# Kernel optimization log

Hardware: AMD Instinct MI355X
Metric: run time of the kernel (lower is better)

Reference implementation:

```python
import jax, jax.numpy as jnp
import numpy as np

B = 4096
HASH_BITS = 128
TEACHER_DIM = 768
TEMPERATURE = 0.2
CONTRASTIVE_W = 1.0
DISTILL_W = 0.5
QUANT_W = 0.01


def _l2_normalize(x, eps=1e-12):
    # matches torch F.normalize(dim=-1)
    n = jnp.sqrt(jnp.sum(x * x, axis=-1, keepdims=True))
    return x / jnp.maximum(n, eps)


def setup_inputs() -> dict:
    key = jax.random.key(0)
    k1, k2, k3, k4 = jax.random.split(key, 4)
    logits = jax.random.normal(k1, (B, HASH_BITS), dtype=jnp.float32)
    # binary {-1,+1} codes as in the module contract
    hash_codes = jnp.sign(jax.random.normal(k2, (B, HASH_BITS), dtype=jnp.float32))
    hash_codes = jnp.where(hash_codes == 0, 1.0, hash_codes)
    teacher_embed = jax.random.normal(k3, (B, TEACHER_DIM), dtype=jnp.float32)
    # sparse random positives plus self-positives (guarantees each row nonempty)
    rand_pos = jax.random.uniform(k4, (B, B)) < 0.002
    eye = jnp.eye(B, dtype=bool)
    positive_mask = rand_pos | eye
    return {
        "logits": logits,
        "hash_codes": hash_codes,
        "teacher_embed": teacher_embed,
        "positive_mask": positive_mask,
    }


def reference(logits, hash_codes, teacher_embed, positive_mask):
    teacher = _l2_normalize(teacher_embed)

    # ---- contrastive (vectorized form of the per-row python loop) ----
    ln = _l2_normalize(logits)
    sim = (ln @ ln.T) / TEMPERATURE  # [B, B]
    eye = jnp.eye(sim.shape[0], dtype=bool)
    sim_masked = jnp.where(eye, -jnp.inf, sim)
    # per-row stable logsumexp over self-masked similarities
    log_denom = jax.nn.logsumexp(sim_masked, axis=1)  # [B]
    pm = positive_mask.astype(sim.dtype)
    cnt = pm.sum(axis=1)  # [B]
    pos_mean = (sim * pm).sum(axis=1) / jnp.maximum(cnt, 1.0)
    has_pos = cnt > 0
    per_row = jnp.where(has_pos, -pos_mean + log_denom, 0.0)
    num_pos = jnp.maximum(has_pos.sum(), 1)
    loss_cont = per_row.sum() / num_pos.astype(sim.dtype)

    # ---- distillation: hash similarity vs teacher similarity MSE ----
    hash_sim = (hash_codes @ hash_codes.T) / hash_codes.shape[-1]
    teacher_sim = teacher @ teacher.T
    loss_distill = jnp.mean((hash_sim - teacher_sim) ** 2)

    # ---- quantization: push |logits| toward 1 ----
    loss_quant = jnp.mean(jnp.abs(jnp.abs(logits) - 1.0))

    total = (
        CONTRASTIVE_W * loss_cont
        + DISTILL_W * loss_distill
        + QUANT_W * loss_quant
    )
    return total
```

## Files before the change

kernel.cpp:

```cpp
#include <hip/hip_runtime.h>


typedef unsigned short u16x8 __attribute__((ext_vector_type(8)));
typedef __bf16 bf16x8 __attribute__((ext_vector_type(8)));
typedef float f32x4 __attribute__((ext_vector_type(4)));

__device__ __forceinline__ unsigned short f2bf(float f) {
  union { float f; unsigned int u; } v; v.f = f;
  unsigned int u = v.u;
  return (unsigned short)((u + 0x7FFFu + ((u >> 16) & 1u)) >> 16);
}

__global__ __launch_bounds__(256) void prep(const float* __restrict__ logits,
                                            const float* __restrict__ hash,
                                            const float* __restrict__ teacher,
                                            unsigned short* __restrict__ P,
                                            float* __restrict__ qpart,
                                            float* __restrict__ rowexp,
                                            float* __restrict__ possum,
                                            float* __restrict__ cntw) {
  const int r = blockIdx.x, t = threadIdx.x;
  const int wave = t >> 6, lane = t & 63;
  __shared__ float s4[4], s2[2], q2[2];

  float x0 = teacher[(size_t)r * 768 + t];
  float x1 = teacher[(size_t)r * 768 + 256 + t];
  float x2 = teacher[(size_t)r * 768 + 512 + t];
  float ss = x0 * x0 + x1 * x1 + x2 * x2;
#pragma unroll
  for (int off = 1; off < 64; off <<= 1) ss += __shfl_xor(ss, off, 64);
  if (lane == 0) s4[wave] = ss;

  float xl = 0.f;
  if (t < 128) {
    xl = logits[(size_t)r * 128 + t];
    float ssl = xl * xl;
    float qv = fabsf(fabsf(xl) - 1.0f);
#pragma unroll
    for (int off = 1; off < 64; off <<= 1) {
      ssl += __shfl_xor(ssl, off, 64);
      qv += __shfl_xor(qv, off, 64);
    }
    if (lane == 0) { s2[wave] = ssl; q2[wave] = qv; }
  }
  __syncthreads();

  float rnt = 1.0f / fmaxf(sqrtf(s4[0] + s4[1] + s4[2] + s4[3]), 1e-12f);
  P[(size_t)r * 1024 + 256 + t] = f2bf(x0 * rnt);
  P[(size_t)r * 1024 + 512 + t] = f2bf(x1 * rnt);
  P[(size_t)r * 1024 + 768 + t] = f2bf(x2 * rnt);
  if (t < 128) {
    float rnl = 1.0f / fmaxf(sqrtf(s2[0] + s2[1]), 1e-12f);
    P[(size_t)r * 1024 + t] = f2bf(xl * rnl);
    P[(size_t)r * 1024 + 128 + t] =
        f2bf(hash[(size_t)r * 128 + t] * 0.08838834764831845f);
  }
  if (t == 0) {
    qpart[r] = q2[0] + q2[1];
    rowexp[r] = 0.f; possum[r] = 0.f; cntw[r] = 0.f;
  }
}

#define STAGE(KC)                                                              \
  {                                                                            \
    _Pragma("unroll") for (int it = 0; it < 4; ++it) {                         \
      const int seg = it * 4 + wave;                                           \
      const int row = seg * 4 + (lane >> 4);                                   \
      const int g = (lane & 15) ^ (row & 7);                                   \
      const unsigned short* gpA =                                              \
          P + (size_t)(ti + row) * 1024 + (KC) * 128 + g * 8;                  \
      __builtin_amdgcn_global_load_lds(                                        \
          (const __attribute__((address_space(1))) void*)gpA,                  \
          (__attribute__((address_space(3))) void*)&S[seg * 512], 16, 0, 0);   \
      if (offdiag) {                                                           \
        const unsigned short* gpB =                                            \
            P + (size_t)(tj + row) * 1024 + (KC) * 128 + g * 8;                \
        __builtin_amdgcn_global_load_lds(                                      \
            (const __attribute__((address_space(1))) void*)gpB,                \
            (__attribute__((address_space(3))) void*)&S[8192 + seg * 512],     \
            16, 0, 0);                                                         \
      }                                                                        \
    }                                                                          \
  }

#define CHUNK_MFMA(A0, A1, A2, A3)                                             \
  {                                                                            \
    _Pragma("unroll") for (int ks = 0; ks < 4; ++ks) {                         \
      const int gg = (ks * 4 + qd) ^ swz;                                      \
      bf16x8 af = *(const bf16x8*)&S[(wave * 16 + l15) * 128 + gg * 8];        \
      bf16x8 b0 = *(const bf16x8*)&S[boff + l15 * 128 + gg * 8];               \
      A0 = __builtin_amdgcn_mfma_f32_16x16x32_bf16(af, b0, A0, 0, 0, 0);       \
      bf16x8 b1 = *(const bf16x8*)&S[boff + (16 + l15) * 128 + gg * 8];        \
      A1 = __builtin_amdgcn_mfma_f32_16x16x32_bf16(af, b1, A1, 0, 0, 0);       \
      bf16x8 b2 = *(const bf16x8*)&S[boff + (32 + l15) * 128 + gg * 8];        \
      A2 = __builtin_amdgcn_mfma_f32_16x16x32_bf16(af, b2, A2, 0, 0, 0);       \
      bf16x8 b3 = *(const bf16x8*)&S[boff + (48 + l15) * 128 + gg * 8];        \
      A3 = __builtin_amdgcn_mfma_f32_16x16x32_bf16(af, b3, A3, 0, 0, 0);       \
    }                                                                          \
  }

__global__ __launch_bounds__(256) void hash_main(const unsigned short* __restrict__ P,
                                                 const void* __restrict__ mask,
                                                 float* __restrict__ rowexp,
                                                 float* __restrict__ possum,
                                                 float* __restrict__ cntw,
                                                 float* __restrict__ dpart) {
  const int b = (int)blockIdx.x;
  const int l = (b & 7) * 260 + (b >> 3);
  int bi = (int)((129.0f - sqrtf(16641.0f - 8.0f * (float)l)) * 0.5f);
  while (bi * (129 - bi) / 2 > l) --bi;
  while ((bi + 1) * (128 - bi) / 2 <= l) ++bi;
  const int bj = bi + (l - bi * (129 - bi) / 2);
  const int ti = bi * 64, tj = bj * 64;
  const bool offdiag = (bi != bj);

  const int t = threadIdx.x;
  const int wave = t >> 6, lane = t & 63;
  const int qd = lane >> 4, l15 = lane & 15;
  const int swz = l15 & 7;

  __shared__ __align__(16) unsigned short S[16384];
  __shared__ float red[4];
  const int boff = offdiag ? 8192 : 0;

  f32x4 s0 = {0.f, 0.f, 0.f, 0.f}, s1 = s0, s2 = s0, s3 = s0;
  f32x4 d0 = s0, d1 = s0, d2 = s0, d3 = s0;

  STAGE(0); __syncthreads(); CHUNK_MFMA(s0, s1, s2, s3);
#pragma unroll
  for (int kc = 2; kc < 8; ++kc) {
    __syncthreads(); STAGE(kc); __syncthreads(); CHUNK_MFMA(d0, d1, d2, d3);
  }
  d0 = -d0; d1 = -d1; d2 = -d2; d3 = -d3;
  __syncthreads(); STAGE(1); __syncthreads();
  CHUNK_MFMA(d0, d1, d2, d3);

  const f32x4 Sv[4] = {s0, s1, s2, s3};
  const f32x4 Dv[4] = {d0, d1, d2, d3};

  __syncthreads();
  unsigned char* MD = (unsigned char*)S;
  unsigned char* MM = (unsigned char*)S + 4096;
  const bool is_byte = ((const unsigned char*)mask)[4097] != 0;
  const unsigned char* m8 = (const unsigned char*)mask;
  const unsigned int* m32 = (const unsigned int*)mask;
  if (is_byte) {
    const int row = t >> 2, seg = t & 3;
    *(uint4*)&MD[row * 64 + seg * 16] =
        *(const uint4*)&m8[(size_t)(ti + row) * 4096 + tj + seg * 16];
    if (offdiag)
      *(uint4*)&MM[row * 64 + seg * 16] =
          *(const uint4*)&m8[(size_t)(tj + row) * 4096 + ti + seg * 16];
  } else {
#pragma unroll
    for (int p = 0; p < 4; ++p) {
      const int unit = t + p * 256;
      const int row = unit >> 4, seg = unit & 15;
      uint4 v = *(const uint4*)&m32[(size_t)(ti + row) * 4096 + tj + seg * 4];
      uchar4 pk;
      pk.x = v.x ? 1 : 0; pk.y = v.y ? 1 : 0; pk.z = v.z ? 1 : 0; pk.w = v.w ? 1 : 0;
      *(uchar4*)&MD[row * 64 + seg * 4] = pk;
      if (offdiag) {
        uint4 w = *(const uint4*)&m32[(size_t)(tj + row) * 4096 + ti + seg * 4];
        uchar4 pm;
        pm.x = w.x ? 1 : 0; pm.y = w.y ? 1 : 0; pm.z = w.z ? 1 : 0; pm.w = w.w ? 1 : 0;
        *(uchar4*)&MM[row * 64 + seg * 4] = pm;
      }
    }
  }
  __syncthreads();

  float dsum = 0.f;
  float colexp[4] = {0.f, 0.f, 0.f, 0.f};
#pragma unroll
  for (int r = 0; r < 4; ++r) {
    const int mrow = wave * 16 + qd * 4 + r;
    const int m = ti + mrow;
    float se = 0.f;
#pragma unroll
    for (int nt = 0; nt < 4; ++nt) {
      const int ncol = nt * 16 + l15;
      const int n = tj + ncol;
      const float sim = Sv[nt][r] * 5.0f;
      const float e = __expf(sim);
      if (offdiag || m != n) se += e;
      if (offdiag) colexp[nt] += e;
      if (MD[mrow * 64 + ncol]) {
        atomicAdd(&possum[m], sim);
        atomicAdd(&cntw[m], 1.0f);
      }
      if (offdiag && MM[ncol * 64 + mrow]) {
        atomicAdd(&possum[n], sim);
        atomicAdd(&cntw[n], 1.0f);
      }
      const float dv = Dv[nt][r];
      dsum += dv * dv;
    }
#pragma unroll
    for (int off = 1; off < 16; off <<= 1) se += __shfl_xor(se, off, 64);
    if (l15 == 0) atomicAdd(&rowexp[m], se);
  }
  if (offdiag) {
#pragma unroll
    for (int nt = 0; nt < 4; ++nt) {
      float ce = colexp[nt];
      ce += __shfl_xor(ce, 16, 64); ce += __shfl_xor(ce, 32, 64);
      if (qd == 0) atomicAdd(&rowexp[tj + nt * 16 + l15], ce);
    }
  }
#pragma unroll
  for (int off = 1; off < 64; off <<= 1) dsum += __shfl_xor(dsum, off, 64);
  if (lane == 0) red[wave] = dsum;
  __syncthreads();
  if (t == 0)
    dpart[l] = (offdiag ? 2.0f : 1.0f) * (red[0] + red[1] + red[2] + red[3]);
}

__global__ __launch_bounds__(1024) void finalize(const float* __restrict__ rowexp,
                                                 const float* __restrict__ possum,
                                                 const float* __restrict__ cnt,
                                                 const float* __restrict__ qpart,
                                                 const float* __restrict__ dpart,
                                                 float* __restrict__ out) {
  const int t = threadIdx.x;
  const int wave = t >> 6, lane = t & 63;
  float c = 0.f, q = 0.f, d = 0.f;
  for (int m = t; m < 4096; m += 1024) {
    c += logf(rowexp[m]) - possum[m] / fmaxf(cnt[m], 1.0f);
    q += qpart[m];
  }
  for (int i = t; i < 2080; i += 1024) d += dpart[i];
#pragma unroll
  for (int off = 1; off < 64; off <<= 1) {
    c += __shfl_xor(c, off, 64);
    q += __shfl_xor(q, off, 64);
    d += __shfl_xor(d, off, 64);
  }
  __shared__ float sc[16], sq[16], sd[16];
  if (lane == 0) { sc[wave] = c; sq[wave] = q; sd[wave] = d; }
  __syncthreads();
  if (t == 0) {
    float C = 0.f, Q = 0.f, D = 0.f;
    for (int i = 0; i < 16; ++i) { C += sc[i]; Q += sq[i]; D += sd[i]; }
    out[0] = C * (1.0f / 4096.0f) + 0.5f * (D * (1.0f / 16777216.0f)) +
             0.01f * (Q * (1.0f / 524288.0f));
  }
}

extern "C" void kernel_launch(void* const* d_in, const int* in_sizes, int n_in,
                              void* d_out, int out_size, void* d_ws, size_t ws_size,
                              hipStream_t stream) {
  const float* logits = (const float*)d_in[0];
  const float* hash = (const float*)d_in[1];
  const float* teacher = (const float*)d_in[2];
  const void* mask = d_in[3];
  float* out = (float*)d_out;

  char* ws = (char*)d_ws;
  float* rowexp = (float*)(ws + 0);
  float* possum = (float*)(ws + 16384);
  float* cntw = (float*)(ws + 32768);
  float* qpart = (float*)(ws + 49152);
  float* dpart = (float*)(ws + 65536);
  unsigned short* P = (unsigned short*)(ws + 98304);

  prep<<<4096, 256, 0, stream>>>(logits, hash, teacher, P, qpart, rowexp, possum, cntw);
  hash_main<<<2080, 256, 0, stream>>>(P, mask, rowexp, possum, cntw, dpart);
  finalize<<<1, 1024, 0, stream>>>(rowexp, possum, cntw, qpart, dpart, out);
}
```

Baseline: 189.6 us.

## Enlarge tiles to 128x128, split contrastive and distill blocks, fuse finalize

```diff
diff --git a/kernel.cpp b/kernel.cpp
--- a/kernel.cpp
+++ b/kernel.cpp
@@ -18,232 +18,283 @@
                                             float* __restrict__ qpart,
                                             float* __restrict__ rowexp,
                                             float* __restrict__ possum,
-                                            float* __restrict__ cntw) {
-  const int r = blockIdx.x, t = threadIdx.x;
-  const int wave = t >> 6, lane = t & 63;
-  __shared__ float s4[4], s2[2], q2[2];
-
-  float x0 = teacher[(size_t)r * 768 + t];
-  float x1 = teacher[(size_t)r * 768 + 256 + t];
-  float x2 = teacher[(size_t)r * 768 + 512 + t];
-  float ss = x0 * x0 + x1 * x1 + x2 * x2;
-#pragma unroll
-  for (int off = 1; off < 64; off <<= 1) ss += __shfl_xor(ss, off, 64);
-  if (lane == 0) s4[wave] = ss;
-
-  float xl = 0.f;
-  if (t < 128) {
-    xl = logits[(size_t)r * 128 + t];
-    float ssl = xl * xl;
-    float qv = fabsf(fabsf(xl) - 1.0f);
-#pragma unroll
-    for (int off = 1; off < 64; off <<= 1) {
-      ssl += __shfl_xor(ssl, off, 64);
-      qv += __shfl_xor(qv, off, 64);
-    }
-    if (lane == 0) { s2[wave] = ssl; q2[wave] = qv; }
-  }
-  __syncthreads();
-
-  float rnt = 1.0f / fmaxf(sqrtf(s4[0] + s4[1] + s4[2] + s4[3]), 1e-12f);
-  P[(size_t)r * 1024 + 256 + t] = f2bf(x0 * rnt);
-  P[(size_t)r * 1024 + 512 + t] = f2bf(x1 * rnt);
-  P[(size_t)r * 1024 + 768 + t] = f2bf(x2 * rnt);
-  if (t < 128) {
-    float rnl = 1.0f / fmaxf(sqrtf(s2[0] + s2[1]), 1e-12f);
-    P[(size_t)r * 1024 + t] = f2bf(xl * rnl);
-    P[(size_t)r * 1024 + 128 + t] =
-        f2bf(hash[(size_t)r * 128 + t] * 0.08838834764831845f);
-  }
-  if (t == 0) {
-    qpart[r] = q2[0] + q2[1];
+                                            float* __restrict__ cntw,
+                                            float* __restrict__ dtot,
+                                            int* __restrict__ done) {
+  const int r = blockIdx.x * 4 + (threadIdx.x >> 6);
+  const int lane = threadIdx.x & 63;
+  float tv[12];
+  float ss = 0.f;
+#pragma unroll
+  for (int i = 0; i < 12; ++i) {
+    tv[i] = teacher[(size_t)r * 768 + i * 64 + lane];
+    ss += tv[i] * tv[i];
+  }
+  const float l0 = logits[(size_t)r * 128 + lane];
+  const float l1 = logits[(size_t)r * 128 + 64 + lane];
+  const float h0 = hash[(size_t)r * 128 + lane];
+  const float h1 = hash[(size_t)r * 128 + 64 + lane];
+  float ssl = l0 * l0 + l1 * l1;
+  float qv = fabsf(fabsf(l0) - 1.f) + fabsf(fabsf(l1) - 1.f);
+#pragma unroll
+  for (int off = 1; off < 64; off <<= 1) {
+    ss += __shfl_xor(ss, off, 64);
+    ssl += __shfl_xor(ssl, off, 64);
+    qv += __shfl_xor(qv, off, 64);
+  }
+  const float rnt = 1.f / fmaxf(sqrtf(ss), 1e-12f);
+  const float rnl = 1.f / fmaxf(sqrtf(ssl), 1e-12f);
+  unsigned short* Pr = P + (size_t)r * 1024;
+  Pr[lane] = f2bf(l0 * rnl);
+  Pr[64 + lane] = f2bf(l1 * rnl);
+  Pr[128 + lane] = f2bf(h0 * 0.08838834764831845f);
+  Pr[192 + lane] = f2bf(h1 * 0.08838834764831845f);
+#pragma unroll
+  for (int i = 0; i < 12; ++i) Pr[256 + i * 64 + lane] = f2bf(tv[i] * rnt);
+  if (lane == 0) {
+    qpart[r] = qv;
     rowexp[r] = 0.f; possum[r] = 0.f; cntw[r] = 0.f;
+    if (r == 0) { *dtot = 0.f; *done = 0; }
   }
 }
 
-#define STAGE(KC)                                                              \
+#define STAGE64(COL0)                                                          \
   {                                                                            \
     _Pragma("unroll") for (int it = 0; it < 4; ++it) {                         \
-      const int seg = it * 4 + wave;                                           \
-      const int row = seg * 4 + (lane >> 4);                                   \
-      const int g = (lane & 15) ^ (row & 7);                                   \
+      const int task = it * 256 + t;                                           \
+      const int row = task >> 3;                                               \
+      const int g = (task & 7) ^ (row & 7);                                    \
       const unsigned short* gpA =                                              \
-          P + (size_t)(ti + row) * 1024 + (KC) * 128 + g * 8;                  \
+          P + (size_t)(ti + row) * 1024 + (COL0) + g * 8;                      \
       __builtin_amdgcn_global_load_lds(                                        \
           (const __attribute__((address_space(1))) void*)gpA,                  \
-          (__attribute__((address_space(3))) void*)&S[seg * 512], 16, 0, 0);   \
+          (__attribute__((address_space(3))) void*)&S[it * 2048 + wave * 512], \
+          16, 0, 0);                                                           \
       if (offdiag) {                                                           \
         const unsigned short* gpB =                                            \
-            P + (size_t)(tj + row) * 1024 + (KC) * 128 + g * 8;                \
+            P + (size_t)(tj + row) * 1024 + (COL0) + g * 8;                    \
         __builtin_amdgcn_global_load_lds(                                      \
             (const __attribute__((address_space(1))) void*)gpB,                \
-            (__attribute__((address_space(3))) void*)&S[8192 + seg * 512],     \
+            (__attribute__((address_space(3)))                                 \
+                 void*)&S[8192 + it * 2048 + wave * 512],                      \
             16, 0, 0);                                                         \
       }                                                                        \
     }                                                                          \
   }
 
-#define CHUNK_MFMA(A0, A1, A2, A3)                                             \
+#define MFMA_CHUNK()                                                           \
   {                                                                            \
-    _Pragma("unroll") for (int ks = 0; ks < 4; ++ks) {                         \
-      const int gg = (ks * 4 + qd) ^ swz;                                      \
-      bf16x8 af = *(const bf16x8*)&S[(wave * 16 + l15) * 128 + gg * 8];        \
-      bf16x8 b0 = *(const bf16x8*)&S[boff + l15 * 128 + gg * 8];               \
-      A0 = __builtin_amdgcn_mfma_f32_16x16x32_bf16(af, b0, A0, 0, 0, 0);       \
-      bf16x8 b1 = *(const bf16x8*)&S[boff + (16 + l15) * 128 + gg * 8];        \
-      A1 = __builtin_amdgcn_mfma_f32_16x16x32_bf16(af, b1, A1, 0, 0, 0);       \
-      bf16x8 b2 = *(const bf16x8*)&S[boff + (32 + l15) * 128 + gg * 8];        \
-      A2 = __builtin_amdgcn_mfma_f32_16x16x32_bf16(af, b2, A2, 0, 0, 0);       \
-      bf16x8 b3 = *(const bf16x8*)&S[boff + (48 + l15) * 128 + gg * 8];        \
-      A3 = __builtin_amdgcn_mfma_f32_16x16x32_bf16(af, b3, A3, 0, 0, 0);       \
+    _Pragma("unroll") for (int ks = 0; ks < 2; ++ks) {                         \
+      bf16x8 af[4], bfr[4];                                                    \
+      _Pragma("unroll") for (int rt = 0; rt < 4; ++rt) {                       \
+        const int ar = wy * 64 + rt * 16 + l15;                                \
+        af[rt] =                                                               \
+            *(const bf16x8*)&S[ar * 64 + ((ks * 4 + qd) ^ (l15 & 7)) * 8];     \
+      }                                                                        \
+      _Pragma("unroll") for (int ct = 0; ct < 4; ++ct) {                       \
+        const int br = wx * 64 + ct * 16 + l15;                                \
+        bfr[ct] = *(const bf16x8*)&S[boff + br * 64 +                          \
+                                     ((ks * 4 + qd) ^ (l15 & 7)) * 8];         \
+      }                                                                        \
+      _Pragma("unroll") for (int rt = 0; rt < 4; ++rt)                         \
+          _Pragma("unroll") for (int ct = 0; ct < 4; ++ct) acc[rt][ct] =       \
+          __builtin_amdgcn_mfma_f32_16x16x32_bf16(af[rt], bfr[ct],             \
+                                                  acc[rt][ct], 0, 0, 0);       \
     }                                                                          \
   }
 
-__global__ __launch_bounds__(256) void hash_main(const unsigned short* __restrict__ P,
-                                                 const void* __restrict__ mask,
-                                                 float* __restrict__ rowexp,
-                                                 float* __restrict__ possum,
-                                                 float* __restrict__ cntw,
-                                                 float* __restrict__ dpart) {
-  const int b = (int)blockIdx.x;
-  const int l = (b & 7) * 260 + (b >> 3);
-  int bi = (int)((129.0f - sqrtf(16641.0f - 8.0f * (float)l)) * 0.5f);
-  while (bi * (129 - bi) / 2 > l) --bi;
-  while ((bi + 1) * (128 - bi) / 2 <= l) ++bi;
-  const int bj = bi + (l - bi * (129 - bi) / 2);
-  const int ti = bi * 64, tj = bj * 64;
-  const bool offdiag = (bi != bj);
+__global__ __launch_bounds__(256, 3) void mega(const unsigned short* __restrict__ P,
+                                               const void* __restrict__ mask,
+                                               float* __restrict__ rowexp,
+                                               float* __restrict__ possum,
+                                               float* __restrict__ cntw,
+                                               float* __restrict__ dtot,
+                                               int* __restrict__ done,
+                                               const float* __restrict__ qpart,
+                                               float* __restrict__ out) {
+  __shared__ __align__(16) unsigned short S[16384];
+  __shared__ float redrow[128][2], redcol[128][2], red4[4];
+  __shared__ float fc[4], fq[4];
+  __shared__ int lastf;
 
   const int t = threadIdx.x;
   const int wave = t >> 6, lane = t & 63;
   const int qd = lane >> 4, l15 = lane & 15;
-  const int swz = l15 & 7;
-
-  __shared__ __align__(16) unsigned short S[16384];
-  __shared__ float red[4];
+  const int wy = wave >> 1, wx = wave & 1;
+
+  const int b = (int)blockIdx.x;
+  const bool isD = b < 528;
+  const int bb = isD ? b : b - 528;
+  const int l = (bb & 7) * 66 + (bb >> 3);
+  int bi = (int)((65.0f - sqrtf(4225.0f - 8.0f * (float)l)) * 0.5f);
+  while (bi * (65 - bi) / 2 > l) --bi;
+  while ((bi + 1) * (64 - bi) / 2 <= l) ++bi;
+  const int bj = bi + (l - bi * (65 - bi) / 2);
+  const int ti = bi * 128, tj = bj * 128;
+  const bool offdiag = (bi != bj);
   const int boff = offdiag ? 8192 : 0;
 
-  f32x4 s0 = {0.f, 0.f, 0.f, 0.f}, s1 = s0, s2 = s0, s3 = s0;
-  f32x4 d0 = s0, d1 = s0, d2 = s0, d3 = s0;
-
-  STAGE(0); __syncthreads(); CHUNK_MFMA(s0, s1, s2, s3);
-#pragma unroll
-  for (int kc = 2; kc < 8; ++kc) {
-    __syncthreads(); STAGE(kc); __syncthreads(); CHUNK_MFMA(d0, d1, d2, d3);
-  }
-  d0 = -d0; d1 = -d1; d2 = -d2; d3 = -d3;
-  __syncthreads(); STAGE(1); __syncthreads();
-  CHUNK_MFMA(d0, d1, d2, d3);
-
-  const f32x4 Sv[4] = {s0, s1, s2, s3};
-  const f32x4 Dv[4] = {d0, d1, d2, d3};
-
+  f32x4 acc[4][4];
+#pragma unroll
+  for (int rt = 0; rt < 4; ++rt)
+#pragma unroll
+    for (int ct = 0; ct < 4; ++ct) acc[rt][ct] = {0.f, 0.f, 0.f, 0.f};
+
+  if (isD) {
+    for (int kc = 0; kc < 14; ++kc) {
+      const int col0 = (kc < 12) ? (256 + kc * 64) : (128 + (kc - 12) * 64);
+      __syncthreads();
+      STAGE64(col0);
+      __syncthreads();
+      if (kc == 12) {
+#pragma unroll
+        for (int rt = 0; rt < 4; ++rt)
+#pragma unroll
+          for (int ct = 0; ct < 4; ++ct) acc[rt][ct] = -acc[rt][ct];
+      }
+      MFMA_CHUNK();
+    }
+    float dsum = 0.f;
+#pragma unroll
+    for (int rt = 0; rt < 4; ++rt)
+#pragma unroll
+      for (int ct = 0; ct < 4; ++ct)
+#pragma unroll
+        for (int i = 0; i < 4; ++i) dsum += acc[rt][ct][i] * acc[rt][ct][i];
+#pragma unroll
+    for (int off = 1; off < 64; off <<= 1) dsum += __shfl_xor(dsum, off, 64);
+    if (lane == 0) red4[wave] = dsum;
+    __syncthreads();
+    if (t == 0)
+      atomicAdd(dtot, (offdiag ? 2.0f : 1.0f) *
+                          (red4[0] + red4[1] + red4[2] + red4[3]));
+  } else {
+    for (int kc = 0; kc < 2; ++kc) {
+      const int col0 = kc * 64;
+      __syncthreads();
+      STAGE64(col0);
+      __syncthreads();
+      MFMA_CHUNK();
+    }
+
+    __syncthreads();
+    unsigned char* MD = (unsigned char*)S;
+    unsigned char* MM = (unsigned char*)S + 16384;
+    const bool is_byte = ((const unsigned char*)mask)[4097] != 0;
+    if (is_byte) {
+      const unsigned char* m8 = (const unsigned char*)mask;
+#pragma unroll
+      for (int it = 0; it < 4; ++it) {
+        const int task = it * 256 + t;
+        const int row = task >> 3, seg = task & 7;
+        *(uint4*)&MD[row * 128 + seg * 16] =
+            *(const uint4*)&m8[(size_t)(ti + row) * 4096 + tj + seg * 16];
+        if (offdiag)
+          *(uint4*)&MM[row * 128 + seg * 16] =
+              *(const uint4*)&m8[(size_t)(tj + row) * 4096 + ti + seg * 16];
+      }
+    } else {
+      const unsigned int* m32 = (const unsigned int*)mask;
+#pragma unroll
+      for (int it = 0; it < 16; ++it) {
+        const int task = it * 256 + t;
+        const int row = task >> 5, seg = task & 31;
+        uint4 v = *(const uint4*)&m32[(size_t)(ti + row) * 4096 + tj + seg * 4];
+        uchar4 pk;
+        pk.x = v.x ? 1 : 0; pk.y = v.y ? 1 : 0;
+        pk.z = v.z ? 1 : 0; pk.w = v.w ? 1 : 0;
+        *(uchar4*)&MD[row * 128 + seg * 4] = pk;
+        if (offdiag) {
+          uint4 w = *(const uint4*)&m32[(size_t)(tj + row) * 4096 + ti + seg * 4];
+          uchar4 pm;
+          pm.x = w.x ? 1 : 0; pm.y = w.y ? 1 : 0;
+          pm.z = w.z ? 1 : 0; pm.w = w.w ? 1 : 0;
+          *(uchar4*)&MM[row * 128 + seg * 4] = pm;
+        }
+      }
+    }
+    __syncthreads();
+
+    float colp[4] = {0.f, 0.f, 0.f, 0.f};
+#pragma unroll
+    for (int rt = 0; rt < 4; ++rt) {
+#pragma unroll
+      for (int r = 0; r < 4; ++r) {
+        const int mrow = wy * 64 + rt * 16 + qd * 4 + r;
+        const int m = ti + mrow;
+        float se = 0.f;
+#pragma unroll
+        for (int ct = 0; ct < 4; ++ct) {
+          const int ncol = wx * 64 + ct * 16 + l15;
+          const int n = tj + ncol;
+          const float sim = acc[rt][ct][r] * 5.0f;
+          const float e = __expf(sim);
+          if (offdiag || mrow != ncol) se += e;
+          if (offdiag) colp[ct] += e;
+          if (MD[mrow * 128 + ncol]) {
+            atomicAdd(&possum[m], sim);
+            atomicAdd(&cntw[m], 1.0f);
+          }
+          if (offdiag && MM[ncol * 128 + mrow]) {
+            atomicAdd(&possum[n], sim);
+            atomicAdd(&cntw[n], 1.0f);
+          }
+        }
+#pragma unroll
+        for (int off = 1; off < 16; off <<= 1) se += __shfl_xor(se, off, 64);
+        if (l15 == 0) redrow[mrow][wx] = se;
+      }
+    }
+    if (offdiag) {
+#pragma unroll
+      for (int ct = 0; ct < 4; ++ct) {
+        float ce = colp[ct];
+        ce += __shfl_xor(ce, 16, 64);
+        ce += __shfl_xor(ce, 32, 64);
+        if (qd == 0) redcol[wx * 64 + ct * 16 + l15][wy] = ce;
+      }
+    }
+    __syncthreads();
+    if (t < 128) {
+      atomicAdd(&rowexp[ti + t], redrow[t][0] + redrow[t][1]);
+      if (offdiag) atomicAdd(&rowexp[tj + t], redcol[t][0] + redcol[t][1]);
+    }
+  }
+
+  __threadfence();
+  if (t == 0) {
+    const int old = __hip_atomic_fetch_add(done, 1, __ATOMIC_ACQ_REL,
+                                           __HIP_MEMORY_SCOPE_AGENT);
+    lastf = (old == 1055) ? 1 : 0;
+  }
   __syncthreads();
-  unsigned char* MD = (unsigned char*)S;
-  unsigned char* MM = (unsigned char*)S + 4096;
-  const bool is_byte = ((const unsigned char*)mask)[4097] != 0;
-  const unsigned char* m8 = (const unsigned char*)mask;
-  const unsigned int* m32 = (const unsigned int*)mask;
-  if (is_byte) {
-    const int row = t >> 2, seg = t & 3;
-    *(uint4*)&MD[row * 64 + seg * 16] =
-        *(const uint4*)&m8[(size_t)(ti + row) * 4096 + tj + seg * 16];
-    if (offdiag)
-      *(uint4*)&MM[row * 64 + seg * 16] =
-          *(const uint4*)&m8[(size_t)(tj + row) * 4096 + ti + seg * 16];
-  } else {
-#pragma unroll
-    for (int p = 0; p < 4; ++p) {
-      const int unit = t + p * 256;
-      const int row = unit >> 4, seg = unit & 15;
-      uint4 v = *(const uint4*)&m32[(size_t)(ti + row) * 4096 + tj + seg * 4];
-      uchar4 pk;
-      pk.x = v.x ? 1 : 0; pk.y = v.y ? 1 : 0; pk.z = v.z ? 1 : 0; pk.w = v.w ? 1 : 0;
-      *(uchar4*)&MD[row * 64 + seg * 4] = pk;
-      if (offdiag) {
-        uint4 w = *(const uint4*)&m32[(size_t)(tj + row) * 4096 + ti + seg * 4];
-        uchar4 pm;
-        pm.x = w.x ? 1 : 0; pm.y = w.y ? 1 : 0; pm.z = w.z ? 1 : 0; pm.w = w.w ? 1 : 0;
-        *(uchar4*)&MM[row * 64 + seg * 4] = pm;
-      }
-    }
-  }
-  __syncthreads();
-
-  float dsum = 0.f;
-  float colexp[4] = {0.f, 0.f, 0.f, 0.f};
-#pragma unroll
-  for (int r = 0; r < 4; ++r) {
-    const int mrow = wave * 16 + qd * 4 + r;
-    const int m = ti + mrow;
-    float se = 0.f;
-#pragma unroll
-    for (int nt = 0; nt < 4; ++nt) {
-      const int ncol = nt * 16 + l15;
-      const int n = tj + ncol;
-      const float sim = Sv[nt][r] * 5.0f;
-      const float e = __expf(sim);
-      if (offdiag || m != n) se += e;
-      if (offdiag) colexp[nt] += e;
-      if (MD[mrow * 64 + ncol]) {
-        atomicAdd(&possum[m], sim);
-        atomicAdd(&cntw[m], 1.0f);
-      }
-      if (offdiag && MM[ncol * 64 + mrow]) {
-        atomicAdd(&possum[n], sim);
-        atomicAdd(&cntw[n], 1.0f);
-      }
-      const float dv = Dv[nt][r];
-      dsum += dv * dv;
-    }
-#pragma unroll
-    for (int off = 1; off < 16; off <<= 1) se += __shfl_xor(se, off, 64);
-    if (l15 == 0) atomicAdd(&rowexp[m], se);
-  }
-  if (offdiag) {
-#pragma unroll
-    for (int nt = 0; nt < 4; ++nt) {
-      float ce = colexp[nt];
-      ce += __shfl_xor(ce, 16, 64); ce += __shfl_xor(ce, 32, 64);
-      if (qd == 0) atomicAdd(&rowexp[tj + nt * 16 + l15], ce);
-    }
-  }
-#pragma unroll
-  for (int off = 1; off < 64; off <<= 1) dsum += __shfl_xor(dsum, off, 64);
-  if (lane == 0) red[wave] = dsum;
-  __syncthreads();
-  if (t == 0)
-    dpart[l] = (offdiag ? 2.0f : 1.0f) * (red[0] + red[1] + red[2] + red[3]);
-}
-
-__global__ __launch_bounds__(1024) void finalize(const float* __restrict__ rowexp,
-                                                 const float* __restrict__ possum,
-                                                 const float* __restrict__ cnt,
-                                                 const float* __restrict__ qpart,
-                                                 const float* __restrict__ dpart,
-                                                 float* __restrict__ out) {
-  const int t = threadIdx.x;
-  const int wave = t >> 6, lane = t & 63;
-  float c = 0.f, q = 0.f, d = 0.f;
-  for (int m = t; m < 4096; m += 1024) {
-    c += logf(rowexp[m]) - possum[m] / fmaxf(cnt[m], 1.0f);
-    q += qpart[m];
-  }
-  for (int i = t; i < 2080; i += 1024) d += dpart[i];
-#pragma unroll
-  for (int off = 1; off < 64; off <<= 1) {
-    c += __shfl_xor(c, off, 64);
-    q += __shfl_xor(q, off, 64);
-    d += __shfl_xor(d, off, 64);
-  }
-  __shared__ float sc[16], sq[16], sd[16];
-  if (lane == 0) { sc[wave] = c; sq[wave] = q; sd[wave] = d; }
-  __syncthreads();
-  if (t == 0) {
-    float C = 0.f, Q = 0.f, D = 0.f;
-    for (int i = 0; i < 16; ++i) { C += sc[i]; Q += sq[i]; D += sd[i]; }
-    out[0] = C * (1.0f / 4096.0f) + 0.5f * (D * (1.0f / 16777216.0f)) +
-             0.01f * (Q * (1.0f / 524288.0f));
+  if (lastf) {
+    float c = 0.f, q = 0.f;
+    for (int m = t; m < 4096; m += 256) {
+      const float re = __hip_atomic_load(&rowexp[m], __ATOMIC_RELAXED,
+                                         __HIP_MEMORY_SCOPE_AGENT);
+      const float ps = __hip_atomic_load(&possum[m], __ATOMIC_RELAXED,
+                                         __HIP_MEMORY_SCOPE_AGENT);
+      const float cn = __hip_atomic_load(&cntw[m], __ATOMIC_RELAXED,
+                                         __HIP_MEMORY_SCOPE_AGENT);
+      c += logf(re) - ps / fmaxf(cn, 1.0f);
+      q += qpart[m];
+    }
+#pragma unroll
+    for (int off = 1; off < 64; off <<= 1) {
+      c += __shfl_xor(c, off, 64);
+      q += __shfl_xor(q, off, 64);
+    }
+    if (lane == 0) { fc[wave] = c; fq[wave] = q; }
+    __syncthreads();
+    if (t == 0) {
+      const float C = fc[0] + fc[1] + fc[2] + fc[3];
+      const float Q = fq[0] + fq[1] + fq[2] + fq[3];
+      const float D = __hip_atomic_load(dtot, __ATOMIC_RELAXED,
+                                        __HIP_MEMORY_SCOPE_AGENT);
+      out[0] = C * (1.0f / 4096.0f) + 0.5f * (D * (1.0f / 16777216.0f)) +
+               0.01f * (Q * (1.0f / 524288.0f));
+    }
   }
 }
 
@@ -261,10 +312,12 @@
   float* possum = (float*)(ws + 16384);
   float* cntw = (float*)(ws + 32768);
   float* qpart = (float*)(ws + 49152);
-  float* dpart = (float*)(ws + 65536);
+  float* dtot = (float*)(ws + 65536);
+  int* done = (int*)(ws + 65544);
   unsigned short* P = (unsigned short*)(ws + 98304);
 
-  prep<<<4096, 256, 0, stream>>>(logits, hash, teacher, P, qpart, rowexp, possum, cntw);
-  hash_main<<<2080, 256, 0, stream>>>(P, mask, rowexp, possum, cntw, dpart);
-  finalize<<<1, 1024, 0, stream>>>(rowexp, possum, cntw, qpart, dpart, out);
+  prep<<<1024, 256, 0, stream>>>(logits, hash, teacher, P, qpart, rowexp,
+                                 possum, cntw, dtot, done);
+  mega<<<1056, 256, 0, stream>>>(P, mask, rowexp, possum, cntw, dtot, done,
+                                 qpart, out);
 }
```

Result: slower. 271.1 us (+43.0%).
